# Kernel optimization log

Hardware: AMD Instinct MI355X
Metric: run time of the kernel (lower is better)

## Reference

```python
import jax, jax.numpy as jnp
import numpy as np

N_NODES = 100000
N_EDGES = 1600000
D = 128
EPS = 1e-5


def setup_inputs() -> dict:
    key = jax.random.key(0)
    k1, k2, k3 = jax.random.split(key, 3)
    x = jax.random.normal(k1, (N_NODES, D), dtype=jnp.float32)
    edge_index = jax.random.randint(k2, (2, N_EDGES), 0, N_NODES, dtype=jnp.int64)
    W = jax.random.normal(k3, (D, D), dtype=jnp.float32) * (1.0 / np.sqrt(D))
    b = jnp.zeros((D,), dtype=jnp.float32)
    gamma = jnp.ones((D,), dtype=jnp.float32)
    beta = jnp.zeros((D,), dtype=jnp.float32)
    return {"x": x, "edge_index": edge_index, "W": W, "b": b, "gamma": gamma, "beta": beta}


def reference(x, edge_index, W, b, gamma, beta):
    N = x.shape[0]
    loops = jnp.arange(N, dtype=edge_index.dtype)
    src = jnp.concatenate([edge_index[0], loops])  # [E+N]
    dst = jnp.concatenate([edge_index[1], loops])  # [E+N]
    # symmetric GCN normalization with self-loops; deg >= 1 always
    deg = jax.ops.segment_sum(jnp.ones_like(dst, dtype=x.dtype), dst, num_segments=N)
    dis = jax.lax.rsqrt(deg)
    xw = x @ W  # [N, D]
    norm = (dis[src] * dis[dst])[:, None]  # [E+N, 1]
    agg = jax.ops.segment_sum(xw[src] * norm, dst, num_segments=N) + b
    h = agg + x  # residual (in_channels == out_channels -> Identity proj)
    mu = jnp.mean(h, axis=-1, keepdims=True)
    var = jnp.mean(jnp.square(h - mu), axis=-1, keepdims=True)
    h = (h - mu) * jax.lax.rsqrt(var + EPS) * gamma + beta
    return jax.nn.relu(h)  # dropout = identity in eval mode
```

## Files before the change

kernel.cpp:

```cpp
#include <hip/hip_runtime.h>
#include <cstdint>
#include <cstddef>

#define NN 100000
#define NE 1600000
#define DD 128
#define EPSV 1e-5f
#define NPART 8
#define PSIZE (NN / NPART)
#define NCHUNK 256
#define CSZ (NE / NCHUNK)

static __device__ inline unsigned short f2bf(float f) {
    unsigned u = __float_as_uint(f);
    unsigned r = (u + 0x7fffu + ((u >> 16) & 1u)) >> 16;
    return (unsigned short)r;
}

static __device__ inline float bflo(unsigned u) { return __uint_as_float(u << 16); }
static __device__ inline float bfhi(unsigned u) { return __uint_as_float(u & 0xffff0000u); }

__global__ void detect_kernel(const unsigned* __restrict__ raw, int* __restrict__ flag) {
    int i = blockIdx.x * blockDim.x + threadIdx.x;
    if (i >= 4096) return;
    size_t idx = (size_t)i * 780 + 1;
    if (raw[idx] != 0) atomicOr(flag, 1);
}

__global__ void convert_kernel(const int* __restrict__ raw, int* __restrict__ e32,
                               const int* __restrict__ flag,
                               const float* __restrict__ x, unsigned short* __restrict__ xb,
                               int* __restrict__ cnt) {
    const int is32 = *flag;
    const int stride = gridDim.x * blockDim.x;
    const int tid0 = blockIdx.x * blockDim.x + threadIdx.x;
    for (int i = tid0; i < 2 * NE; i += stride) {
        const int v = is32 ? raw[i] : raw[2 * (size_t)i];
        e32[i] = v;
        if (i >= NE) atomicAdd(&cnt[v], 1);
    }
    for (int i = tid0; i < NN * DD / 4; i += stride) {
        const float4 v = *(const float4*)(x + (size_t)i * 4);
        ushort4 o;
        o.x = f2bf(v.x); o.y = f2bf(v.y); o.z = f2bf(v.z); o.w = f2bf(v.w);
        *(ushort4*)(xb + (size_t)i * 4) = o;
    }
}

__global__ void alloc_kernel(const int* __restrict__ cnt, int* __restrict__ start,
                             int* __restrict__ fill, float* __restrict__ dis,
                             int* __restrict__ cursor) {
    __shared__ int sdata[256];
    __shared__ int sbase;
    const int tid = threadIdx.x;
    const int v = blockIdx.x * 256 + tid;
    const int c = (v < NN) ? cnt[v] : 0;
    sdata[tid] = c;
    __syncthreads();
    #pragma unroll
    for (int off = 1; off < 256; off <<= 1) {
        int t = (tid >= off) ? sdata[tid - off] : 0;
        __syncthreads();
        sdata[tid] += t;
        __syncthreads();
    }
    const int excl = sdata[tid] - c;
    const int total = sdata[255];
    if (tid == 0) sbase = atomicAdd(cursor, total);
    __syncthreads();
    if (v < NN) {
        const int st = sbase + excl;
        start[v] = st;
        fill[v] = st;
        dis[v] = rsqrtf((float)(c + 1));
    }
}

__global__ void scatter_kernel(const int* __restrict__ e32, int* __restrict__ fill,
                               int* __restrict__ ssrc) {
    const int part = blockIdx.x & (NPART - 1);
    const int chunk = blockIdx.x >> 3;
    const int lo = part * PSIZE, hi = lo + PSIZE;
    const int e0 = chunk * CSZ, e1 = e0 + CSZ;
    for (int e = e0 + threadIdx.x; e < e1; e += 256) {
        const int d = e32[NE + e];
        if (d >= lo && d < hi) {
            const int s = e32[e];
            const int p = atomicAdd(&fill[d], 1);
            ssrc[p] = s;
        }
    }
}

__global__ void agg_kernel(const unsigned short* __restrict__ xb,
                           const int* __restrict__ ssrc, const int* __restrict__ start,
                           const int* __restrict__ cnt, const float* __restrict__ dis,
                           unsigned short* __restrict__ agg) {
    const int wave = threadIdx.x >> 6, lane = threadIdx.x & 63;
    const int node = blockIdx.x * 4 + wave;
    if (node >= NN) return;
    const float dv = dis[node];
    const unsigned us = *(const unsigned*)(xb + (size_t)node * DD + 2 * lane);
    float accx = dv * dv * bflo(us);
    float accy = dv * dv * bfhi(us);
    const int s0 = start[node];
    const int c = cnt[node];
    for (int chunk = 0; chunk < c; chunk += 64) {
        const int rem0 = c - chunk;
        const int rem = rem0 < 64 ? rem0 : 64;
        int sj = 0; float dsj = 0.f;
        if (lane < rem) {
            sj = ssrc[s0 + chunk + lane];
            dsj = dis[sj];
        }
        int j = 0;
        for (; j + 4 <= rem; j += 4) {
            const int i0 = __builtin_amdgcn_readlane(sj, j);
            const int i1 = __builtin_amdgcn_readlane(sj, j + 1);
            const int i2 = __builtin_amdgcn_readlane(sj, j + 2);
            const int i3 = __builtin_amdgcn_readlane(sj, j + 3);
            const float w0 = __uint_as_float(__builtin_amdgcn_readlane(__float_as_uint(dsj), j)) * dv;
            const float w1 = __uint_as_float(__builtin_amdgcn_readlane(__float_as_uint(dsj), j + 1)) * dv;
            const float w2 = __uint_as_float(__builtin_amdgcn_readlane(__float_as_uint(dsj), j + 2)) * dv;
            const float w3 = __uint_as_float(__builtin_amdgcn_readlane(__float_as_uint(dsj), j + 3)) * dv;
            const unsigned v0 = *(const unsigned*)(xb + (size_t)i0 * DD + 2 * lane);
            const unsigned v1 = *(const unsigned*)(xb + (size_t)i1 * DD + 2 * lane);
            const unsigned v2 = *(const unsigned*)(xb + (size_t)i2 * DD + 2 * lane);
            const unsigned v3 = *(const unsigned*)(xb + (size_t)i3 * DD + 2 * lane);
            accx = fmaf(w0, bflo(v0), accx); accy = fmaf(w0, bfhi(v0), accy);
            accx = fmaf(w1, bflo(v1), accx); accy = fmaf(w1, bfhi(v1), accy);
            accx = fmaf(w2, bflo(v2), accx); accy = fmaf(w2, bfhi(v2), accy);
            accx = fmaf(w3, bflo(v3), accx); accy = fmaf(w3, bfhi(v3), accy);
        }
        for (; j < rem; ++j) {
            const int s = __builtin_amdgcn_readlane(sj, j);
            const float w = __uint_as_float(__builtin_amdgcn_readlane(__float_as_uint(dsj), j)) * dv;
            const unsigned uv = *(const unsigned*)(xb + (size_t)s * DD + 2 * lane);
            accx = fmaf(w, bflo(uv), accx);
            accy = fmaf(w, bfhi(uv), accy);
        }
    }
    ushort2 st; st.x = f2bf(accx); st.y = f2bf(accy);
    *(ushort2*)(agg + (size_t)node * DD + 2 * lane) = st;
}

__global__ __launch_bounds__(256) void gemm2_kernel(const unsigned short* __restrict__ agg,
                                                    const float* __restrict__ x,
                                                    const float* __restrict__ W,
                                                    const float* __restrict__ b,
                                                    const float* __restrict__ g,
                                                    const float* __restrict__ be,
                                                    float* __restrict__ out) {
    __shared__ float Wl[DD * DD];
    __shared__ float Al[32 * DD];
    const int tid = threadIdx.x;
    for (int i = tid * 4; i < DD * DD; i += 1024)
        *(float4*)(Wl + i) = *(const float4*)(W + i);
    const int wave = tid >> 6, lane = tid & 63;
    const float2 bb = *(const float2*)(b + 2 * lane);
    const float2 gg = *(const float2*)(g + 2 * lane);
    const float2 bt = *(const float2*)(be + 2 * lane);
    for (int grp = blockIdx.x; grp < NN / 32; grp += gridDim.x) {
        const size_t base = (size_t)grp * 32;
        __syncthreads();
        for (int i = tid * 4; i < 32 * DD; i += 1024) {
            const ushort4 u = *(const ushort4*)(agg + base * DD + i);
            float4 v;
            v.x = __uint_as_float((unsigned)u.x << 16);
            v.y = __uint_as_float((unsigned)u.y << 16);
            v.z = __uint_as_float((unsigned)u.z << 16);
            v.w = __uint_as_float((unsigned)u.w << 16);
            *(float4*)(Al + i) = v;
        }
        __syncthreads();
        float ax[8], ay[8];
        #pragma unroll
        for (int r = 0; r < 8; ++r) { ax[r] = 0.f; ay[r] = 0.f; }
        const float* Arow = Al + wave * 8 * DD;
        for (int k = 0; k < DD; k += 4) {
            const float2 w0 = *(const float2*)(Wl + (k + 0) * DD + 2 * lane);
            const float2 w1 = *(const float2*)(Wl + (k + 1) * DD + 2 * lane);
            const float2 w2 = *(const float2*)(Wl + (k + 2) * DD + 2 * lane);
            const float2 w3 = *(const float2*)(Wl + (k + 3) * DD + 2 * lane);
            #pragma unroll
            for (int r = 0; r < 8; ++r) {
                const float4 xv = *(const float4*)(Arow + r * DD + k);
                ax[r] = fmaf(xv.x, w0.x, ax[r]); ay[r] = fmaf(xv.x, w0.y, ay[r]);
                ax[r] = fmaf(xv.y, w1.x, ax[r]); ay[r] = fmaf(xv.y, w1.y, ay[r]);
                ax[r] = fmaf(xv.z, w2.x, ax[r]); ay[r] = fmaf(xv.z, w2.y, ay[r]);
                ax[r] = fmaf(xv.w, w3.x, ax[r]); ay[r] = fmaf(xv.w, w3.y, ay[r]);
            }
        }
        #pragma unroll
        for (int r = 0; r < 8; ++r) {
            const size_t row = base + wave * 8 + r;
            const float2 xr = *(const float2*)(x + row * DD + 2 * lane);
            const float h0 = ax[r] + bb.x + xr.x;
            const float h1 = ay[r] + bb.y + xr.y;
            float sum = h0 + h1;
            #pragma unroll
            for (int off = 32; off; off >>= 1) sum += __shfl_xor(sum, off);
            const float mu = sum * (1.f / 128.f);
            const float e0 = h0 - mu, e1 = h1 - mu;
            float s2 = e0 * e0 + e1 * e1;
            #pragma unroll
            for (int off = 32; off; off >>= 1) s2 += __shfl_xor(s2, off);
            const float inv = rsqrtf(s2 * (1.f / 128.f) + EPSV);
            float2 o;
            o.x = fmaxf(0.f, e0 * inv * gg.x + bt.x);
            o.y = fmaxf(0.f, e1 * inv * gg.y + bt.y);
            *(float2*)(out + row * DD + 2 * lane) = o;
        }
    }
}

extern "C" void kernel_launch(void* const* d_in, const int* in_sizes, int n_in,
                              void* d_out, int out_size, void* d_ws, size_t ws_size,
                              hipStream_t stream) {
    const float* x  = (const float*)d_in[0];
    const int*   ei = (const int*)d_in[1];
    const float* W  = (const float*)d_in[2];
    const float* b  = (const float*)d_in[3];
    const float* g  = (const float*)d_in[4];
    const float* be = (const float*)d_in[5];
    float* out = (float*)d_out;

    char* ws = (char*)d_ws;
    size_t off = 0;
    unsigned short* xb  = (unsigned short*)(ws + off); off += (size_t)NN * DD * 2;
    unsigned short* agg = (unsigned short*)(ws + off); off += (size_t)NN * DD * 2;
    int*   e32   = (int*)(ws + off);   off += (size_t)2 * NE * 4;
    int*   ssrc  = (int*)(ws + off);   off += (size_t)NE * 4;
    int*   cnt   = (int*)(ws + off);   off += (size_t)NN * 4;
    int*   start = (int*)(ws + off);   off += (size_t)NN * 4;
    int*   fill  = (int*)(ws + off);   off += (size_t)NN * 4;
    float* dis   = (float*)(ws + off); off += (size_t)NN * 4;
    int*   flagc = (int*)(ws + off);   off += 256;

    hipMemsetAsync(cnt, 0, (size_t)NN * 4, stream);
    hipMemsetAsync(flagc, 0, 256, stream);

    detect_kernel<<<16, 256, 0, stream>>>((const unsigned*)ei, flagc);
    convert_kernel<<<2048, 256, 0, stream>>>(ei, e32, flagc, x, xb, cnt);
    alloc_kernel<<<(NN + 255) / 256, 256, 0, stream>>>(cnt, start, fill, dis, flagc + 1);
    scatter_kernel<<<NPART * NCHUNK, 256, 0, stream>>>(e32, fill, ssrc);
    agg_kernel<<<NN / 4, 256, 0, stream>>>(xb, ssrc, start, cnt, dis, agg);
    gemm2_kernel<<<512, 256, 0, stream>>>(agg, x, W, b, g, be, out);
}
```

Measured before the change: 401.6 us.

## Use bf16 MFMA for the final GEMM and read the bf16 residual

Rewrites the final GEMM + LayerNorm kernel to use 16x16x32 bf16 MFMA instructions. W is pre-converted to bf16 in the convert kernel, and its fragments are held in registers per wave. The fp32 shared-memory FMA GEMM and its LDS staging are removed. The residual now comes from the bf16 copy of x instead of fp32 x, which halves that read but lowers residual precision. The LayerNorm row reductions are redone for the MFMA output layout, and output stores become 16-lane-strided scalar writes.

```diff
diff --git a/kernel.cpp b/kernel.cpp
--- a/kernel.cpp
+++ b/kernel.cpp
@@ -11,6 +11,9 @@
 #define NCHUNK 256
 #define CSZ (NE / NCHUNK)
 
+typedef __attribute__((ext_vector_type(8))) short bf16x8;
+typedef __attribute__((ext_vector_type(4))) float f32x4;
+
 static __device__ inline unsigned short f2bf(float f) {
     unsigned u = __float_as_uint(f);
     unsigned r = (u + 0x7fffu + ((u >> 16) & 1u)) >> 16;
@@ -30,6 +33,7 @@
 __global__ void convert_kernel(const int* __restrict__ raw, int* __restrict__ e32,
                                const int* __restrict__ flag,
                                const float* __restrict__ x, unsigned short* __restrict__ xb,
+                               const float* __restrict__ W, unsigned short* __restrict__ wb,
                                int* __restrict__ cnt) {
     const int is32 = *flag;
     const int stride = gridDim.x * blockDim.x;
@@ -44,6 +48,12 @@
         ushort4 o;
         o.x = f2bf(v.x); o.y = f2bf(v.y); o.z = f2bf(v.z); o.w = f2bf(v.w);
         *(ushort4*)(xb + (size_t)i * 4) = o;
+    }
+    for (int i = tid0; i < DD * DD / 4; i += stride) {
+        const float4 v = *(const float4*)(W + (size_t)i * 4);
+        ushort4 o;
+        o.x = f2bf(v.x); o.y = f2bf(v.y); o.z = f2bf(v.z); o.w = f2bf(v.w);
+        *(ushort4*)(wb + (size_t)i * 4) = o;
     }
 }
 
@@ -145,71 +155,86 @@
 }
 
 __global__ __launch_bounds__(256) void gemm2_kernel(const unsigned short* __restrict__ agg,
-                                                    const float* __restrict__ x,
-                                                    const float* __restrict__ W,
+                                                    const unsigned short* __restrict__ xb,
+                                                    const unsigned short* __restrict__ wb,
                                                     const float* __restrict__ b,
                                                     const float* __restrict__ g,
                                                     const float* __restrict__ be,
                                                     float* __restrict__ out) {
-    __shared__ float Wl[DD * DD];
-    __shared__ float Al[32 * DD];
-    const int tid = threadIdx.x;
-    for (int i = tid * 4; i < DD * DD; i += 1024)
-        *(float4*)(Wl + i) = *(const float4*)(W + i);
-    const int wave = tid >> 6, lane = tid & 63;
-    const float2 bb = *(const float2*)(b + 2 * lane);
-    const float2 gg = *(const float2*)(g + 2 * lane);
-    const float2 bt = *(const float2*)(be + 2 * lane);
-    for (int grp = blockIdx.x; grp < NN / 32; grp += gridDim.x) {
-        const size_t base = (size_t)grp * 32;
-        __syncthreads();
-        for (int i = tid * 4; i < 32 * DD; i += 1024) {
-            const ushort4 u = *(const ushort4*)(agg + base * DD + i);
-            float4 v;
-            v.x = __uint_as_float((unsigned)u.x << 16);
-            v.y = __uint_as_float((unsigned)u.y << 16);
-            v.z = __uint_as_float((unsigned)u.z << 16);
-            v.w = __uint_as_float((unsigned)u.w << 16);
-            *(float4*)(Al + i) = v;
-        }
-        __syncthreads();
-        float ax[8], ay[8];
-        #pragma unroll
-        for (int r = 0; r < 8; ++r) { ax[r] = 0.f; ay[r] = 0.f; }
-        const float* Arow = Al + wave * 8 * DD;
-        for (int k = 0; k < DD; k += 4) {
-            const float2 w0 = *(const float2*)(Wl + (k + 0) * DD + 2 * lane);
-            const float2 w1 = *(const float2*)(Wl + (k + 1) * DD + 2 * lane);
-            const float2 w2 = *(const float2*)(Wl + (k + 2) * DD + 2 * lane);
-            const float2 w3 = *(const float2*)(Wl + (k + 3) * DD + 2 * lane);
-            #pragma unroll
-            for (int r = 0; r < 8; ++r) {
-                const float4 xv = *(const float4*)(Arow + r * DD + k);
-                ax[r] = fmaf(xv.x, w0.x, ax[r]); ay[r] = fmaf(xv.x, w0.y, ay[r]);
-                ax[r] = fmaf(xv.y, w1.x, ax[r]); ay[r] = fmaf(xv.y, w1.y, ay[r]);
-                ax[r] = fmaf(xv.z, w2.x, ax[r]); ay[r] = fmaf(xv.z, w2.y, ay[r]);
-                ax[r] = fmaf(xv.w, w3.x, ax[r]); ay[r] = fmaf(xv.w, w3.y, ay[r]);
+    const int wave = threadIdx.x >> 6, lane = threadIdx.x & 63;
+    const int grp = lane >> 4;
+    const int lc  = lane & 15;
+    bf16x8 bfr[4][8];
+    #pragma unroll
+    for (int kb = 0; kb < 4; ++kb) {
+        #pragma unroll
+        for (int t = 0; t < 8; ++t) {
+            bf16x8 v;
+            #pragma unroll
+            for (int j = 0; j < 8; ++j)
+                v[j] = (short)wb[(size_t)(kb * 32 + grp * 8 + j) * DD + t * 16 + lc];
+            bfr[kb][t] = v;
+        }
+    }
+    float bbv[8], ggv[8], btv[8];
+    #pragma unroll
+    for (int t = 0; t < 8; ++t) {
+        bbv[t] = b[t * 16 + lc];
+        ggv[t] = g[t * 16 + lc];
+        btv[t] = be[t * 16 + lc];
+    }
+    const int nrb = NN / 16;
+    const int nw = gridDim.x * 4;
+    for (int rb = blockIdx.x * 4 + wave; rb < nrb; rb += nw) {
+        const unsigned short* ap = agg + (size_t)(rb * 16 + lc) * DD + grp * 8;
+        f32x4 acc[8];
+        #pragma unroll
+        for (int t = 0; t < 8; ++t) acc[t] = (f32x4){0.f, 0.f, 0.f, 0.f};
+        #pragma unroll
+        for (int kb = 0; kb < 4; ++kb) {
+            const bf16x8 a = *(const bf16x8*)(ap + kb * 32);
+            #pragma unroll
+            for (int t = 0; t < 8; ++t)
+                acc[t] = __builtin_amdgcn_mfma_f32_16x16x32_bf16(a, bfr[kb][t], acc[t], 0, 0, 0);
+        }
+        const int r0 = rb * 16 + grp * 4;
+        float h[8][4];
+        float rs[4] = {0.f, 0.f, 0.f, 0.f};
+        #pragma unroll
+        for (int reg = 0; reg < 4; ++reg) {
+            #pragma unroll
+            for (int t = 0; t < 8; ++t) {
+                const unsigned xr = xb[(size_t)(r0 + reg) * DD + t * 16 + lc];
+                const float hv = acc[t][reg] + bbv[t] + bflo(xr);
+                h[t][reg] = hv;
+                rs[reg] += hv;
             }
         }
         #pragma unroll
-        for (int r = 0; r < 8; ++r) {
-            const size_t row = base + wave * 8 + r;
-            const float2 xr = *(const float2*)(x + row * DD + 2 * lane);
-            const float h0 = ax[r] + bb.x + xr.x;
-            const float h1 = ay[r] + bb.y + xr.y;
-            float sum = h0 + h1;
-            #pragma unroll
-            for (int off = 32; off; off >>= 1) sum += __shfl_xor(sum, off);
-            const float mu = sum * (1.f / 128.f);
-            const float e0 = h0 - mu, e1 = h1 - mu;
-            float s2 = e0 * e0 + e1 * e1;
-            #pragma unroll
-            for (int off = 32; off; off >>= 1) s2 += __shfl_xor(s2, off);
-            const float inv = rsqrtf(s2 * (1.f / 128.f) + EPSV);
-            float2 o;
-            o.x = fmaxf(0.f, e0 * inv * gg.x + bt.x);
-            o.y = fmaxf(0.f, e1 * inv * gg.y + bt.y);
-            *(float2*)(out + row * DD + 2 * lane) = o;
+        for (int reg = 0; reg < 4; ++reg) {
+            #pragma unroll
+            for (int off = 8; off; off >>= 1) rs[reg] += __shfl_xor(rs[reg], off);
+        }
+        float mu[4], s2[4] = {0.f, 0.f, 0.f, 0.f};
+        #pragma unroll
+        for (int reg = 0; reg < 4; ++reg) {
+            mu[reg] = rs[reg] * (1.f / 128.f);
+            #pragma unroll
+            for (int t = 0; t < 8; ++t) {
+                const float e = h[t][reg] - mu[reg];
+                s2[reg] += e * e;
+            }
+            #pragma unroll
+            for (int off = 8; off; off >>= 1) s2[reg] += __shfl_xor(s2[reg], off);
+        }
+        #pragma unroll
+        for (int reg = 0; reg < 4; ++reg) {
+            const float inv = rsqrtf(s2[reg] * (1.f / 128.f) + EPSV);
+            #pragma unroll
+            for (int t = 0; t < 8; ++t) {
+                const float o = fmaxf(0.f, (h[t][reg] - mu[reg]) * inv * ggv[t] + btv[t]);
+                out[(size_t)(r0 + reg) * DD + t * 16 + lc] = o;
+            }
         }
     }
 }
@@ -231,6 +256,7 @@
     unsigned short* agg = (unsigned short*)(ws + off); off += (size_t)NN * DD * 2;
     int*   e32   = (int*)(ws + off);   off += (size_t)2 * NE * 4;
     int*   ssrc  = (int*)(ws + off);   off += (size_t)NE * 4;
+    unsigned short* wb = (unsigned short*)(ws + off); off += (size_t)DD * DD * 2;
     int*   cnt   = (int*)(ws + off);   off += (size_t)NN * 4;
     int*   start = (int*)(ws + off);   off += (size_t)NN * 4;
     int*   fill  = (int*)(ws + off);   off += (size_t)NN * 4;
@@ -241,9 +267,9 @@
     hipMemsetAsync(flagc, 0, 256, stream);
 
     detect_kernel<<<16, 256, 0, stream>>>((const unsigned*)ei, flagc);
-    convert_kernel<<<2048, 256, 0, stream>>>(ei, e32, flagc, x, xb, cnt);
+    convert_kernel<<<2048, 256, 0, stream>>>(ei, e32, flagc, x, xb, W, wb, cnt);
     alloc_kernel<<<(NN + 255) / 256, 256, 0, stream>>>(cnt, start, fill, dis, flagc + 1);
     scatter_kernel<<<NPART * NCHUNK, 256, 0, stream>>>(e32, fill, ssrc);
     agg_kernel<<<NN / 4, 256, 0, stream>>>(xb, ssrc, start, cnt, dis, agg);
-    gemm2_kernel<<<512, 256, 0, stream>>>(agg, x, W, b, g, be, out);
-}
+    gemm2_kernel<<<512, 256, 0, stream>>>(agg, xb, wb, b, g, be, out);
+}
```

Measured after the change: 347.1 us. -13.6%, faster.
